# Performance work log

Measured on AMD Instinct MI355X. Metric: run time of the kernel, lower is better.

## Reference

```python
import jax, jax.numpy as jnp
import numpy as np

B, T, C = 4, 2048, 2048
H = 16
D = C // H  # 128


def setup_inputs() -> dict:
    key = jax.random.key(0)
    ks = jax.random.split(key, 9)
    s = 0.02
    return {
        "x": jax.random.normal(ks[0], (B, T, C), dtype=jnp.float32),
        "wq": jax.random.normal(ks[1], (C, C), dtype=jnp.float32) * s,
        "bq": jax.random.normal(ks[2], (C,), dtype=jnp.float32) * s,
        "wk": jax.random.normal(ks[3], (C, C), dtype=jnp.float32) * s,
        "bk": jax.random.normal(ks[4], (C,), dtype=jnp.float32) * s,
        "wv": jax.random.normal(ks[5], (C, C), dtype=jnp.float32) * s,
        "bv": jax.random.normal(ks[6], (C,), dtype=jnp.float32) * s,
        "wo": jax.random.normal(ks[7], (C, C), dtype=jnp.float32) * s,
        "bo": jax.random.normal(ks[8], (C,), dtype=jnp.float32) * s,
    }


def reference(x, wq, bq, wk, bk, wv, bv, wo, bo):
    Bz, Tz, Cz = x.shape
    # projections (torch Linear: x @ W^T + b)
    q = (x @ wq.T + bq).reshape(Bz, Tz, H, D).transpose(0, 2, 1, 3)  # [B,H,T,D]
    k = (x @ wk.T + bk).reshape(Bz, Tz, H, D).transpose(0, 2, 1, 3)
    v = (x @ wv.T + bv).reshape(Bz, Tz, H, D).transpose(0, 2, 1, 3)
    scale = 1.0 / jnp.sqrt(jnp.float32(D))
    scores = jnp.einsum("bhqd,bhkd->bhqk", q, k) * scale  # [B,H,T,T]
    causal = jnp.tril(jnp.ones((Tz, Tz), dtype=bool))
    scores = jnp.where(causal, scores, jnp.float32(-jnp.inf))
    att = jax.nn.softmax(scores, axis=-1)
    out = jnp.einsum("bhqk,bhkd->bhqd", att, v)  # [B,H,T,D]
    out = out.transpose(0, 2, 1, 3).reshape(Bz, Tz, Cz)
    out = out @ wo.T + bo
    return out
```

## Files before the change

kernel.cpp:

```cpp
#include <hip/hip_runtime.h>
#include <hip/hip_bf16.h>

typedef float  f32x4  __attribute__((ext_vector_type(4)));
typedef __bf16 bf16x8 __attribute__((ext_vector_type(8)));
typedef __bf16 bf16x4 __attribute__((ext_vector_type(4)));

#define Bz 4
#define Tz 2048
#define Cz 2048
#define Hh 16
#define Dd 128
#define Mm 8192

__device__ __forceinline__ void gload_lds16(const __bf16* g, __bf16* l) {
  __builtin_amdgcn_global_load_lds(
      (const __attribute__((address_space(1))) void*)g,
      (__attribute__((address_space(3))) void*)l, 16, 0, 0);
}

__global__ __launch_bounds__(256)
void cvt_bf16(const float* __restrict__ in, __bf16* __restrict__ out, int n8) {
  int i = blockIdx.x * 256 + threadIdx.x;
  if (i >= n8) return;
  size_t base = (size_t)i * 8;
  f32x4 a = *(const f32x4*)(in + base);
  f32x4 b = *(const f32x4*)(in + base + 4);
  bf16x8 o;
  o[0]=(__bf16)a[0]; o[1]=(__bf16)a[1]; o[2]=(__bf16)a[2]; o[3]=(__bf16)a[3];
  o[4]=(__bf16)b[0]; o[5]=(__bf16)b[1]; o[6]=(__bf16)b[2]; o[7]=(__bf16)b[3];
  *(bf16x8*)(out + base) = o;
}

__global__ __launch_bounds__(256)
void cvt_w4(const float* __restrict__ w0, const float* __restrict__ w1,
            const float* __restrict__ w2, const float* __restrict__ w3,
            __bf16* __restrict__ wqkv, __bf16* __restrict__ wob) {
  const int n8 = Cz * Cz / 8;
  int i = blockIdx.x * 256 + threadIdx.x;
  if (i >= n8) return;
  const int which = blockIdx.y;
  const float* src = which == 0 ? w0 : which == 1 ? w1 : which == 2 ? w2 : w3;
  __bf16* dst = which == 3 ? wob : wqkv + (size_t)which * Cz * Cz;
  size_t base = (size_t)i * 8;
  f32x4 a = *(const f32x4*)(src + base);
  f32x4 b = *(const f32x4*)(src + base + 4);
  bf16x8 o;
  o[0]=(__bf16)a[0]; o[1]=(__bf16)a[1]; o[2]=(__bf16)a[2]; o[3]=(__bf16)a[3];
  o[4]=(__bf16)b[0]; o[5]=(__bf16)b[1]; o[6]=(__bf16)b[2]; o[7]=(__bf16)b[3];
  *(bf16x8*)(dst + base) = o;
}

__global__ __launch_bounds__(256, 3)
void gemm_qkv(const __bf16* __restrict__ A, const __bf16* __restrict__ W,
              const float* __restrict__ bq, const float* __restrict__ bk,
              const float* __restrict__ bv,
              __bf16* __restrict__ qb, __bf16* __restrict__ kb,
              __bf16* __restrict__ vb, float qscale)
{
  __shared__ __bf16 As[128 * 64];
  __shared__ __bf16 Bs[128 * 64];

  const int tid  = threadIdx.x;
  const int lane = tid & 63;
  const int wave = tid >> 6;
  const int wm = wave >> 1, wn = wave & 1;
  const int g  = lane >> 4;
  const int lr = lane & 15;
  const int row0 = blockIdx.x * 128;
  const int col0 = blockIdx.y * 128;

  const int srow = lane >> 3;
  const int sblk = lane & 7;

  f32x4 acc[4][4] = {};

  for (int kt = 0; kt < Cz; kt += 64) {
    __syncthreads();
    #pragma unroll
    for (int p = 0; p < 4; ++p) {
      const int rb = p * 32 + wave * 8;
      const int r  = rb + srow;
      const int cb = sblk ^ (r & 7);
      gload_lds16(A + (size_t)(row0 + r) * Cz + kt + cb * 8, As + rb * 64);
      gload_lds16(W + (size_t)(col0 + r) * Cz + kt + cb * 8, Bs + rb * 64);
    }
    __syncthreads();
    #pragma unroll
    for (int kk = 0; kk < 2; ++kk) {
      bf16x8 af[4], bfr[4];
      #pragma unroll
      for (int i = 0; i < 4; ++i) {
        const int ar = wm * 64 + i * 16 + lr;
        af[i]  = *(const bf16x8*)(As + ar * 64 + ((((kk<<2)|g) ^ (ar & 7)) << 3));
        const int br = wn * 64 + i * 16 + lr;
        bfr[i] = *(const bf16x8*)(Bs + br * 64 + ((((kk<<2)|g) ^ (br & 7)) << 3));
      }
      #pragma unroll
      for (int i = 0; i < 4; ++i)
        #pragma unroll
        for (int j = 0; j < 4; ++j)
          acc[i][j] = __builtin_amdgcn_mfma_f32_16x16x32_bf16(af[i], bfr[j], acc[i][j], 0, 0, 0);
    }
  }

  const int seg  = col0 >> 11;
  const int csg0 = col0 & 2047;
  const float* bias = seg == 0 ? bq : (seg == 1 ? bk : bv);
  const float scl   = seg == 0 ? qscale : 1.0f;
  __bf16* outp      = seg == 0 ? qb : (seg == 1 ? kb : vb);

  #pragma unroll
  for (int j = 0; j < 4; ++j) {
    const int col = csg0 + wn * 64 + j * 16 + lr;
    const float bvv = bias[col];
    #pragma unroll
    for (int i = 0; i < 4; ++i) {
      if (seg == 2) {
        const int row = row0 + wm * 64 + i * 16 + g * 4;
        const int b = row >> 11, t = row & (Tz - 1);
        const int h = col >> 7,  d = col & (Dd - 1);
        bf16x4 v4;
        #pragma unroll
        for (int r = 0; r < 4; ++r) v4[r] = (__bf16)(acc[i][j][r] + bvv);
        *(bf16x4*)(outp + ((size_t)(b * Hh + h) * Dd + d) * Tz + t) = v4;
      } else {
        #pragma unroll
        for (int r = 0; r < 4; ++r) {
          const int row = row0 + wm * 64 + i * 16 + g * 4 + r;
          const int b = row >> 11, t = row & (Tz - 1);
          const int h = col >> 7,  d = col & (Dd - 1);
          outp[((size_t)(b * Hh + h) * Tz + t) * Dd + d] = (__bf16)((acc[i][j][r] + bvv) * scl);
        }
      }
    }
  }
}

__global__ __launch_bounds__(256, 3)
void gemm_o(const __bf16* __restrict__ A, const __bf16* __restrict__ W,
            const float* __restrict__ bias, float* __restrict__ Out)
{
  __shared__ __bf16 As[128 * 64];
  __shared__ __bf16 Bs[128 * 64];

  const int tid  = threadIdx.x;
  const int lane = tid & 63;
  const int wave = tid >> 6;
  const int wm = wave >> 1, wn = wave & 1;
  const int g  = lane >> 4;
  const int lr = lane & 15;
  const int row0 = blockIdx.x * 128;
  const int col0 = blockIdx.y * 128;

  const int srow = lane >> 3;
  const int sblk = lane & 7;

  f32x4 acc[4][4] = {};

  for (int kt = 0; kt < Cz; kt += 64) {
    __syncthreads();
    #pragma unroll
    for (int p = 0; p < 4; ++p) {
      const int rb = p * 32 + wave * 8;
      const int r  = rb + srow;
      const int cb = sblk ^ (r & 7);
      gload_lds16(A + (size_t)(row0 + r) * Cz + kt + cb * 8, As + rb * 64);
      gload_lds16(W + (size_t)(col0 + r) * Cz + kt + cb * 8, Bs + rb * 64);
    }
    __syncthreads();
    #pragma unroll
    for (int kk = 0; kk < 2; ++kk) {
      bf16x8 af[4], bfr[4];
      #pragma unroll
      for (int i = 0; i < 4; ++i) {
        const int ar = wm * 64 + i * 16 + lr;
        af[i]  = *(const bf16x8*)(As + ar * 64 + ((((kk<<2)|g) ^ (ar & 7)) << 3));
        const int br = wn * 64 + i * 16 + lr;
        bfr[i] = *(const bf16x8*)(Bs + br * 64 + ((((kk<<2)|g) ^ (br & 7)) << 3));
      }
      #pragma unroll
      for (int i = 0; i < 4; ++i)
        #pragma unroll
        for (int j = 0; j < 4; ++j)
          acc[i][j] = __builtin_amdgcn_mfma_f32_16x16x32_bf16(af[i], bfr[j], acc[i][j], 0, 0, 0);
    }
  }

  #pragma unroll
  for (int j = 0; j < 4; ++j) {
    const int col = col0 + wn * 64 + j * 16 + lr;
    const float bvv = bias[col];
    #pragma unroll
    for (int i = 0; i < 4; ++i)
      #pragma unroll
      for (int r = 0; r < 4; ++r) {
        const int row = row0 + wm * 64 + i * 16 + g * 4 + r;
        Out[(size_t)row * Cz + col] = acc[i][j][r] + bvv;
      }
  }
}

__global__ __launch_bounds__(256, 2)
void attn_fwd(const __bf16* __restrict__ Q, const __bf16* __restrict__ Kg,
              const __bf16* __restrict__ Vt, __bf16* __restrict__ O)
{
  __shared__ __bf16 Ks[2][64 * 128];
  __shared__ __bf16 Vs[2][128 * 64];
  __shared__ __bf16 Ps[4][32 * 64];

  const int tid  = threadIdx.x;
  const int lane = tid & 63;
  const int wave = tid >> 6;
  const int g  = lane >> 4;
  const int lr = lane & 15;
  const int pair = blockIdx.x;
  const int bx   = blockIdx.y;
  const int b = pair >> 4, h = pair & 15;

  const __bf16* Qp = Q  + (size_t)pair * Tz * Dd;
  const __bf16* Kp = Kg + (size_t)pair * Tz * Dd;
  const __bf16* Vp = Vt + (size_t)pair * Dd * Tz;

  #define STAGE_KV(kv0_, buf_)                                                  \
    {                                                                           \
      const int kv0s = (kv0_);                                                  \
      _Pragma("unroll")                                                         \
      for (int p = 0; p < 4; ++p) {                                             \
        const int r  = p * 16 + wave * 4 + (lane >> 4);                         \
        const int cb = (lane & 15) ^ (r & 7);                                   \
        gload_lds16(Kp + (size_t)(kv0s + r) * Dd + cb * 8,                      \
                    &Ks[buf_][p * 2048 + wave * 512]);                          \
        const int d  = p * 32 + wave * 8 + (lane >> 3);                         \
        const int cv = (lane & 7) ^ (d & 7);                                    \
        gload_lds16(Vp + (size_t)d * Tz + kv0s + cv * 8,                        \
                    &Vs[buf_][p * 2048 + wave * 512]);                          \
      }                                                                         \
    }

  for (int pass = 0; pass < 2; ++pass) {
    const int qt  = pass == 0 ? (15 - bx) : bx;
    const int qw0 = qt * 128 + wave * 32;

    bf16x8 qf[2][4];
    #pragma unroll
    for (int im = 0; im < 2; ++im)
      #pragma unroll
      for (int ks = 0; ks < 4; ++ks)
        qf[im][ks] = *(const bf16x8*)(Qp + (size_t)(qw0 + im*16 + lr) * Dd + ks*32 + g*8);

    f32x4 oacc[2][8] = {};
    float mrow[2], lsum[2];
    mrow[0] = mrow[1] = -1e30f;
    lsum[0] = lsum[1] = 0.f;

    const int ntiles = 2 * qt + 2;

    STAGE_KV(0, 0);
    __syncthreads();

    for (int kt = 0; kt < ntiles; ++kt) {
      const int cur = kt & 1;
      const int kv0 = kt * 64;
      if (kt + 1 < ntiles) STAGE_KV((kt + 1) * 64, cur ^ 1);

      if (kv0 <= qw0 + 31) {
        f32x4 sacc[2][4] = {};
        __builtin_amdgcn_s_setprio(1);
        #pragma unroll
        for (int ks = 0; ks < 4; ++ks) {
          bf16x8 kf[4];
          #pragma unroll
          for (int in = 0; in < 4; ++in) {
            const int r = in*16 + lr;
            kf[in] = *(const bf16x8*)(&Ks[cur][r * 128 + ((((ks<<2)|g) ^ (r & 7)) << 3)]);
          }
          #pragma unroll
          for (int im = 0; im < 2; ++im)
            #pragma unroll
            for (int in = 0; in < 4; ++in)
              sacc[im][in] = __builtin_amdgcn_mfma_f32_16x16x32_bf16(kf[in], qf[im][ks], sacc[im][in], 0, 0, 0);
        }
        __builtin_amdgcn_s_setprio(0);

        if (kv0 + 63 > qw0) {
          #pragma unroll
          for (int im = 0; im < 2; ++im) {
            const int q = qw0 + im*16 + lr;
            #pragma unroll
            for (int in = 0; in < 4; ++in)
              #pragma unroll
              for (int r = 0; r < 4; ++r) {
                const int kv = kv0 + in*16 + g*4 + r;
                if (kv > q) sacc[im][in][r] = -3e38f;
              }
          }
        }

        #pragma unroll
        for (int im = 0; im < 2; ++im) {
          float m = fmaxf(fmaxf(sacc[im][0][0], sacc[im][0][1]),
                          fmaxf(sacc[im][0][2], sacc[im][0][3]));
          #pragma unroll
          for (int in = 1; in < 4; ++in)
            m = fmaxf(m, fmaxf(fmaxf(sacc[im][in][0], sacc[im][in][1]),
                               fmaxf(sacc[im][in][2], sacc[im][in][3])));
          m = fmaxf(m, __shfl_xor(m, 16));
          m = fmaxf(m, __shfl_xor(m, 32));

          const bool need = m > mrow[im] + 11.54f;
          if (__any(need)) {
            const float mn   = need ? m : mrow[im];
            const float corr = __builtin_amdgcn_exp2f(mrow[im] - mn);
            mrow[im] = mn;
            lsum[im] *= corr;
            const int sb = 20 * g;
            const float c0 = __shfl(corr, sb + 0);
            const float c1 = __shfl(corr, sb + 1);
            const float c2 = __shfl(corr, sb + 2);
            const float c3 = __shfl(corr, sb + 3);
            #pragma unroll
            for (int dn = 0; dn < 8; ++dn) {
              oacc[im][dn][0] *= c0; oacc[im][dn][1] *= c1;
              oacc[im][dn][2] *= c2; oacc[im][dn][3] *= c3;
            }
          }

          float rs = 0.f;
          const int prow = im*16 + lr;
          #pragma unroll
          for (int in = 0; in < 4; ++in) {
            const float p0 = __builtin_amdgcn_exp2f(sacc[im][in][0] - mrow[im]);
            const float p1 = __builtin_amdgcn_exp2f(sacc[im][in][1] - mrow[im]);
            const float p2 = __builtin_amdgcn_exp2f(sacc[im][in][2] - mrow[im]);
            const float p3 = __builtin_amdgcn_exp2f(sacc[im][in][3] - mrow[im]);
            rs += (p0 + p1) + (p2 + p3);
            bf16x4 q4;
            q4[0] = (__bf16)p0; q4[1] = (__bf16)p1;
            q4[2] = (__bf16)p2; q4[3] = (__bf16)p3;
            const int bs = (in*4 + g) ^ ((prow & 3) << 2);
            *(bf16x4*)(&Ps[wave][prow * 64 + bs * 4]) = q4;
          }
          rs += __shfl_xor(rs, 16);
          rs += __shfl_xor(rs, 32);
          lsum[im] += rs;
        }

        __builtin_amdgcn_s_setprio(1);
        #pragma unroll
        for (int kk = 0; kk < 2; ++kk) {
          bf16x8 pa[2];
          #pragma unroll
          for (int im = 0; im < 2; ++im) {
            const int prow = im*16 + lr;
            const int bs = (kk*8 + 2*g) ^ ((prow & 3) << 2);
            pa[im] = *(const bf16x8*)(&Ps[wave][prow * 64 + bs * 4]);
          }
          #pragma unroll
          for (int dn = 0; dn < 8; ++dn) {
            const int d = dn*16 + lr;
            bf16x8 vb = *(const bf16x8*)(&Vs[cur][d * 64 + ((((kk<<2)|g) ^ (d & 7)) << 3)]);
            #pragma unroll
            for (int im = 0; im < 2; ++im)
              oacc[im][dn] = __builtin_amdgcn_mfma_f32_16x16x32_bf16(pa[im], vb, oacc[im][dn], 0, 0, 0);
          }
        }
        __builtin_amdgcn_s_setprio(0);
      }
      __syncthreads();
    }

    #pragma unroll
    for (int im = 0; im < 2; ++im) {
      const float inv = 1.0f / lsum[im];
      const int sb = 20 * g;
      const float i0 = __shfl(inv, sb + 0);
      const float i1 = __shfl(inv, sb + 1);
      const float i2 = __shfl(inv, sb + 2);
      const float i3 = __shfl(inv, sb + 3);
      #pragma unroll
      for (int dn = 0; dn < 8; ++dn) {
        const int qrow = qw0 + im*16 + g*4;
        const int d    = h * Dd + dn*16 + lr;
        O[((size_t)(b * Tz + qrow + 0)) * Cz + d] = (__bf16)(oacc[im][dn][0] * i0);
        O[((size_t)(b * Tz + qrow + 1)) * Cz + d] = (__bf16)(oacc[im][dn][1] * i1);
        O[((size_t)(b * Tz + qrow + 2)) * Cz + d] = (__bf16)(oacc[im][dn][2] * i2);
        O[((size_t)(b * Tz + qrow + 3)) * Cz + d] = (__bf16)(oacc[im][dn][3] * i3);
      }
    }
  }
  #undef STAGE_KV
}

extern "C" void kernel_launch(void* const* d_in, const int* in_sizes, int n_in,
                              void* d_out, int out_size, void* d_ws, size_t ws_size,
                              hipStream_t stream) {
  const float* x  = (const float*)d_in[0];
  const float* wq = (const float*)d_in[1];
  const float* bq = (const float*)d_in[2];
  const float* wk = (const float*)d_in[3];
  const float* bk = (const float*)d_in[4];
  const float* wv = (const float*)d_in[5];
  const float* bv = (const float*)d_in[6];
  const float* wo = (const float*)d_in[7];
  const float* bo = (const float*)d_in[8];
  float* out = (float*)d_out;

  char* w = (char*)d_ws;
  __bf16* xb   = (__bf16*)w; w += (size_t)Mm * Cz * 2;
  __bf16* wob  = (__bf16*)w; w += (size_t)Cz * Cz * 2;
  __bf16* qb   = (__bf16*)w; w += (size_t)Mm * Cz * 2;
  __bf16* kb   = (__bf16*)w; w += (size_t)Mm * Cz * 2;
  __bf16* vbuf = (__bf16*)w; w += (size_t)Mm * Cz * 2;
  if (ws_size < (size_t)(w - (char*)d_ws)) return;

  __bf16* wqkv = (__bf16*)d_out;

  const int nx8 = Mm * Cz / 8;
  const int nw8 = Cz * Cz / 8;
  const float qscale = 0.12752551286084110f;

  cvt_bf16<<<nx8 / 256, 256, 0, stream>>>(x, xb, nx8);
  cvt_w4<<<dim3(nw8 / 256, 4), 256, 0, stream>>>(wq, wk, wv, wo, wqkv, wob);

  gemm_qkv<<<dim3(Mm / 128, 48), 256, 0, stream>>>(xb, wqkv, bq, bk, bv,
                                                   qb, kb, vbuf, qscale);

  __bf16* ob = xb;
  attn_fwd<<<dim3(Bz * Hh, 8), 256, 0, stream>>>(qb, kb, vbuf, ob);

  gemm_o<<<dim3(Mm / 128, Cz / 128), 256, 0, stream>>>(ob, wob, bo, out);
}
```

Before: 385.5 us.

## Split attention work across 8 waves with 16 query rows each

The attention kernel now runs 512 threads per block, 8 waves each handling 16 query rows instead of 4 waves with 32 rows. K/V staging is redistributed across all threads and per-wave P scratch is resized. This halves per-wave register state to raise occupancy and latency hiding. The cost is that each K/V fragment read from LDS now feeds half as many MFMAs, which raises LDS traffic per FLOP, and more waves contend at every barrier.

```diff
diff --git a/kernel.cpp b/kernel.cpp
--- a/kernel.cpp
+++ b/kernel.cpp
@@ -200,13 +200,13 @@
   }
 }
 
-__global__ __launch_bounds__(256, 2)
+__global__ __launch_bounds__(512, 4)
 void attn_fwd(const __bf16* __restrict__ Q, const __bf16* __restrict__ Kg,
               const __bf16* __restrict__ Vt, __bf16* __restrict__ O)
 {
   __shared__ __bf16 Ks[2][64 * 128];
   __shared__ __bf16 Vs[2][128 * 64];
-  __shared__ __bf16 Ps[4][32 * 64];
+  __shared__ __bf16 Ps[8][16 * 64];
 
   const int tid  = threadIdx.x;
   const int lane = tid & 63;
@@ -225,33 +225,29 @@
     {                                                                           \
       const int kv0s = (kv0_);                                                  \
       _Pragma("unroll")                                                         \
-      for (int p = 0; p < 4; ++p) {                                             \
-        const int r  = p * 16 + wave * 4 + (lane >> 4);                         \
-        const int cb = (lane & 15) ^ (r & 7);                                   \
+      for (int p = 0; p < 2; ++p) {                                             \
+        const int r  = p * 32 + (tid >> 4);                                     \
+        const int cb = (tid & 15) ^ (r & 7);                                    \
         gload_lds16(Kp + (size_t)(kv0s + r) * Dd + cb * 8,                      \
-                    &Ks[buf_][p * 2048 + wave * 512]);                          \
-        const int d  = p * 32 + wave * 8 + (lane >> 3);                         \
-        const int cv = (lane & 7) ^ (d & 7);                                    \
+                    &Ks[buf_][p * 4096 + wave * 512]);                          \
+        const int d  = p * 64 + (tid >> 3);                                     \
+        const int cv = (tid & 7) ^ (d & 7);                                     \
         gload_lds16(Vp + (size_t)d * Tz + kv0s + cv * 8,                        \
-                    &Vs[buf_][p * 2048 + wave * 512]);                          \
+                    &Vs[buf_][p * 4096 + wave * 512]);                          \
       }                                                                         \
     }
 
   for (int pass = 0; pass < 2; ++pass) {
     const int qt  = pass == 0 ? (15 - bx) : bx;
-    const int qw0 = qt * 128 + wave * 32;
-
-    bf16x8 qf[2][4];
-    #pragma unroll
-    for (int im = 0; im < 2; ++im)
-      #pragma unroll
-      for (int ks = 0; ks < 4; ++ks)
-        qf[im][ks] = *(const bf16x8*)(Qp + (size_t)(qw0 + im*16 + lr) * Dd + ks*32 + g*8);
-
-    f32x4 oacc[2][8] = {};
-    float mrow[2], lsum[2];
-    mrow[0] = mrow[1] = -1e30f;
-    lsum[0] = lsum[1] = 0.f;
+    const int qw0 = qt * 128 + wave * 16;
+
+    bf16x8 qf[4];
+    #pragma unroll
+    for (int ks = 0; ks < 4; ++ks)
+      qf[ks] = *(const bf16x8*)(Qp + (size_t)(qw0 + lr) * Dd + ks*32 + g*8);
+
+    f32x4 oacc[8] = {};
+    float mrow = -1e30f, lsum = 0.f;
 
     const int ntiles = 2 * qt + 2;
 
@@ -263,8 +259,8 @@
       const int kv0 = kt * 64;
       if (kt + 1 < ntiles) STAGE_KV((kt + 1) * 64, cur ^ 1);
 
-      if (kv0 <= qw0 + 31) {
-        f32x4 sacc[2][4] = {};
+      if (kv0 <= qw0 + 15) {
+        f32x4 sacc[4] = {};
         __builtin_amdgcn_s_setprio(1);
         #pragma unroll
         for (int ks = 0; ks < 4; ++ks) {
@@ -275,44 +271,38 @@
             kf[in] = *(const bf16x8*)(&Ks[cur][r * 128 + ((((ks<<2)|g) ^ (r & 7)) << 3)]);
           }
           #pragma unroll
-          for (int im = 0; im < 2; ++im)
-            #pragma unroll
-            for (int in = 0; in < 4; ++in)
-              sacc[im][in] = __builtin_amdgcn_mfma_f32_16x16x32_bf16(kf[in], qf[im][ks], sacc[im][in], 0, 0, 0);
+          for (int in = 0; in < 4; ++in)
+            sacc[in] = __builtin_amdgcn_mfma_f32_16x16x32_bf16(kf[in], qf[ks], sacc[in], 0, 0, 0);
         }
         __builtin_amdgcn_s_setprio(0);
 
         if (kv0 + 63 > qw0) {
-          #pragma unroll
-          for (int im = 0; im < 2; ++im) {
-            const int q = qw0 + im*16 + lr;
+          const int q = qw0 + lr;
+          #pragma unroll
+          for (int in = 0; in < 4; ++in)
             #pragma unroll
-            for (int in = 0; in < 4; ++in)
-              #pragma unroll
-              for (int r = 0; r < 4; ++r) {
-                const int kv = kv0 + in*16 + g*4 + r;
-                if (kv > q) sacc[im][in][r] = -3e38f;
-              }
-          }
+            for (int r = 0; r < 4; ++r) {
+              const int kv = kv0 + in*16 + g*4 + r;
+              if (kv > q) sacc[in][r] = -3e38f;
+            }
         }
 
-        #pragma unroll
-        for (int im = 0; im < 2; ++im) {
-          float m = fmaxf(fmaxf(sacc[im][0][0], sacc[im][0][1]),
-                          fmaxf(sacc[im][0][2], sacc[im][0][3]));
+        {
+          float m = fmaxf(fmaxf(sacc[0][0], sacc[0][1]),
+                          fmaxf(sacc[0][2], sacc[0][3]));
           #pragma unroll
           for (int in = 1; in < 4; ++in)
-            m = fmaxf(m, fmaxf(fmaxf(sacc[im][in][0], sacc[im][in][1]),
-                               fmaxf(sacc[im][in][2], sacc[im][in][3])));
+            m = fmaxf(m, fmaxf(fmaxf(sacc[in][0], sacc[in][1]),
+                               fmaxf(sacc[in][2], sacc[in][3])));
           m = fmaxf(m, __shfl_xor(m, 16));
           m = fmaxf(m, __shfl_xor(m, 32));
 
-          const bool need = m > mrow[im] + 11.54f;
+          const bool need = m > mrow + 11.54f;
           if (__any(need)) {
-            const float mn   = need ? m : mrow[im];
-            const float corr = __builtin_amdgcn_exp2f(mrow[im] - mn);
-            mrow[im] = mn;
-            lsum[im] *= corr;
+            const float mn   = need ? m : mrow;
+            const float corr = __builtin_amdgcn_exp2f(mrow - mn);
+            mrow = mn;
+            lsum *= corr;
             const int sb = 20 * g;
             const float c0 = __shfl(corr, sb + 0);
             const float c1 = __shfl(corr, sb + 1);
@@ -320,19 +310,19 @@
             const float c3 = __shfl(corr, sb + 3);
             #pragma unroll
             for (int dn = 0; dn < 8; ++dn) {
-              oacc[im][dn][0] *= c0; oacc[im][dn][1] *= c1;
-              oacc[im][dn][2] *= c2; oacc[im][dn][3] *= c3;
+              oacc[dn][0] *= c0; oacc[dn][1] *= c1;
+              oacc[dn][2] *= c2; oacc[dn][3] *= c3;
             }
           }
 
           float rs = 0.f;
-          const int prow = im*16 + lr;
+          const int prow = lr;
           #pragma unroll
           for (int in = 0; in < 4; ++in) {
-            const float p0 = __builtin_amdgcn_exp2f(sacc[im][in][0] - mrow[im]);
-            const float p1 = __builtin_amdgcn_exp2f(sacc[im][in][1] - mrow[im]);
-            const float p2 = __builtin_amdgcn_exp2f(sacc[im][in][2] - mrow[im]);
-            const float p3 = __builtin_amdgcn_exp2f(sacc[im][in][3] - mrow[im]);
+            const float p0 = __builtin_amdgcn_exp2f(sacc[in][0] - mrow);
+            const float p1 = __builtin_amdgcn_exp2f(sacc[in][1] - mrow);
+            const float p2 = __builtin_amdgcn_exp2f(sacc[in][2] - mrow);
+            const float p3 = __builtin_amdgcn_exp2f(sacc[in][3] - mrow);
             rs += (p0 + p1) + (p2 + p3);
             bf16x4 q4;
             q4[0] = (__bf16)p0; q4[1] = (__bf16)p1;
@@ -342,26 +332,20 @@
           }
           rs += __shfl_xor(rs, 16);
           rs += __shfl_xor(rs, 32);
-          lsum[im] += rs;
+          lsum += rs;
         }
 
         __builtin_amdgcn_s_setprio(1);
         #pragma unroll
         for (int kk = 0; kk < 2; ++kk) {
-          bf16x8 pa[2];
-          #pragma unroll
-          for (int im = 0; im < 2; ++im) {
-            const int prow = im*16 + lr;
-            const int bs = (kk*8 + 2*g) ^ ((prow & 3) << 2);
-            pa[im] = *(const bf16x8*)(&Ps[wave][prow * 64 + bs * 4]);
-          }
+          const int prow = lr;
+          const int bs = (kk*8 + 2*g) ^ ((prow & 3) << 2);
+          bf16x8 pa = *(const bf16x8*)(&Ps[wave][prow * 64 + bs * 4]);
           #pragma unroll
           for (int dn = 0; dn < 8; ++dn) {
             const int d = dn*16 + lr;
             bf16x8 vb = *(const bf16x8*)(&Vs[cur][d * 64 + ((((kk<<2)|g) ^ (d & 7)) << 3)]);
-            #pragma unroll
-            for (int im = 0; im < 2; ++im)
-              oacc[im][dn] = __builtin_amdgcn_mfma_f32_16x16x32_bf16(pa[im], vb, oacc[im][dn], 0, 0, 0);
+            oacc[dn] = __builtin_amdgcn_mfma_f32_16x16x32_bf16(pa, vb, oacc[dn], 0, 0, 0);
           }
         }
         __builtin_amdgcn_s_setprio(0);
@@ -369,9 +353,8 @@
       __syncthreads();
     }
 
-    #pragma unroll
-    for (int im = 0; im < 2; ++im) {
-      const float inv = 1.0f / lsum[im];
+    {
+      const float inv = 1.0f / lsum;
       const int sb = 20 * g;
       const float i0 = __shfl(inv, sb + 0);
       const float i1 = __shfl(inv, sb + 1);
@@ -379,12 +362,12 @@
       const float i3 = __shfl(inv, sb + 3);
       #pragma unroll
       for (int dn = 0; dn < 8; ++dn) {
-        const int qrow = qw0 + im*16 + g*4;
+        const int qrow = qw0 + g*4;
         const int d    = h * Dd + dn*16 + lr;
-        O[((size_t)(b * Tz + qrow + 0)) * Cz + d] = (__bf16)(oacc[im][dn][0] * i0);
-        O[((size_t)(b * Tz + qrow + 1)) * Cz + d] = (__bf16)(oacc[im][dn][1] * i1);
-        O[((size_t)(b * Tz + qrow + 2)) * Cz + d] = (__bf16)(oacc[im][dn][2] * i2);
-        O[((size_t)(b * Tz + qrow + 3)) * Cz + d] = (__bf16)(oacc[im][dn][3] * i3);
+        O[((size_t)(b * Tz + qrow + 0)) * Cz + d] = (__bf16)(oacc[dn][0] * i0);
+        O[((size_t)(b * Tz + qrow + 1)) * Cz + d] = (__bf16)(oacc[dn][1] * i1);
+        O[((size_t)(b * Tz + qrow + 2)) * Cz + d] = (__bf16)(oacc[dn][2] * i2);
+        O[((size_t)(b * Tz + qrow + 3)) * Cz + d] = (__bf16)(oacc[dn][3] * i3);
       }
     }
   }
@@ -426,7 +409,7 @@
                                                    qb, kb, vbuf, qscale);
 
   __bf16* ob = xb;
-  attn_fwd<<<dim3(Bz * Hh, 8), 256, 0, stream>>>(qb, kb, vbuf, ob);
+  attn_fwd<<<dim3(Bz * Hh, 8), 512, 0, stream>>>(qb, kb, vbuf, ob);
 
   gemm_o<<<dim3(Mm / 128, Cz / 128), 256, 0, stream>>>(ob, wob, bo, out);
 }
```

Measured after the change: 396.0 us. 1.03x slower.
